# Optimization experiments

Measured on AMD Instinct MI355X. Metric: run time of the kernel, lower is better.

The kernel has to match this reference:

```python
import jax, jax.numpy as jnp
import numpy as np

N_NODES = 50000
N_EDGES = 800000
D_IN = 96
D_HID = 96
D_OUT = 4


def _glorot(key, shape):
    lim = float(np.sqrt(6.0 / (shape[0] + shape[1])))
    return jax.random.uniform(key, shape, jnp.float32, -lim, lim)


def setup_inputs() -> dict:
    key = jax.random.key(0)
    ks = jax.random.split(key, 8)
    x = jax.random.normal(ks[0], (N_NODES, D_IN), jnp.float32)
    edge_index = jax.random.randint(ks[1], (2, N_EDGES), 0, N_NODES, jnp.int64)
    return {
        'x': x,
        'edge_index': edge_index,
        'W0': _glorot(ks[2], (D_IN, D_HID)), 'b0': jnp.zeros((D_HID,), jnp.float32),
        'W1': _glorot(ks[3], (D_HID, D_HID)), 'b1': jnp.zeros((D_HID,), jnp.float32),
        'W2': _glorot(ks[4], (D_HID, D_HID)), 'b2': jnp.zeros((D_HID,), jnp.float32),
        'Wfc': _glorot(ks[5], (D_HID, D_OUT)), 'bfc': jnp.zeros((D_OUT,), jnp.float32),
    }


def _gcn_conv(x, src, dst, W, b, n):
    # GCNConv: linear transform, add self-loops, symmetric degree norm, scatter-add.
    h = x @ W                                   # [N, D]
    loops = jnp.arange(n, dtype=src.dtype)
    s = jnp.concatenate([src, loops])           # [E+N]
    d = jnp.concatenate([dst, loops])
    deg = jax.ops.segment_sum(jnp.ones_like(d, dtype=h.dtype), d, num_segments=n)
    dinv = jnp.where(deg > 0, jax.lax.rsqrt(deg), 0.0)
    norm = dinv[s] * dinv[d]                    # [E+N]
    msgs = h[s] * norm[:, None]                 # gather + scale
    out = jax.ops.segment_sum(msgs, d, num_segments=n)  # scatter-add
    return out + b


def reference(x, edge_index, W0, b0, W1, b1, W2, b2, Wfc, bfc):
    src, dst = edge_index[0], edge_index[1]
    n = x.shape[0]
    h = jax.nn.relu(_gcn_conv(x, src, dst, W0, b0, n))   # dropout = identity (eval)
    h = jax.nn.relu(_gcn_conv(h, src, dst, W1, b1, n))
    h = jax.nn.relu(_gcn_conv(h, src, dst, W2, b2, n))
    return h @ Wfc + bfc
```

## Files before the change

kernel.cpp:

```cpp
#include <hip/hip_runtime.h>

typedef __bf16 bf16x8 __attribute__((ext_vector_type(8)));
typedef float  f32x4  __attribute__((ext_vector_type(4)));
typedef float  f32x8  __attribute__((ext_vector_type(8)));
typedef unsigned short ushort;
typedef ushort us8 __attribute__((ext_vector_type(8)));

constexpr int N_NODES = 50000;
constexpr int N_EDGES = 800000;
constexpr int SLOTS = 64;
constexpr int GE   = N_EDGES / 256;
constexpr int WBLK = (3 * 9216) / 256;
constexpr int GMF  = (N_NODES + 63) / 64;

__device__ inline float h16f(ushort u) {
    union { _Float16 h; ushort u; } cv; cv.u = u; return (float)cv.h;
}
__device__ inline ushort f16b(float f) {
    union { _Float16 h; ushort u; } cv; cv.h = (_Float16)f; return cv.u;
}
__device__ inline ushort bf16b(float f) {
    union { __bf16 b; ushort u; } cv; cv.b = (__bf16)f; return cv.u;
}
__device__ inline f32x8 bf8_to_f32(us8 u) {
    f32x8 r;
#pragma unroll
    for (int i = 0; i < 8; ++i) r[i] = __uint_as_float(((unsigned int)u[i]) << 16);
    return r;
}

__global__ __launch_bounds__(256) void k_count(const int* __restrict__ dst,
                                               int* __restrict__ cnt,
                                               ushort* __restrict__ rank,
                                               const float* __restrict__ W0,
                                               const float* __restrict__ W1,
                                               const float* __restrict__ W2,
                                               ushort* __restrict__ Wt) {
    const int b = blockIdx.x;
    if (b < GE) {
        int e = b * 256 + threadIdx.x;
        rank[e] = (ushort)atomicAdd(&cnt[dst[e]], 1);
    } else {
        int i = (b - GE) * 256 + threadIdx.x;
        int m = i / 9216, li = i - m * 9216;
        const float* W = (m == 0) ? W0 : (m == 1) ? W1 : W2;
        int k = li / 96, c = li - k * 96;
        Wt[m * 9216 + c * 96 + k] = bf16b(W[li]);
    }
}

template<int IN>
__device__ __forceinline__ void gemm_tile(ushort* sX, ushort* sW, const void* Xv,
                                          const ushort* __restrict__ Wt,
                                          ushort* __restrict__ Y, int bt) {
    const int tid = threadIdx.x;
    const int rowbase = bt * 64;

    for (int i = tid; i < 9216 / 8; i += 256)
        ((uint4*)sW)[i] = ((const uint4*)Wt)[i];

    if (IN == 0) {
        const float* X = (const float*)Xv;
        for (int i = tid; i < 64 * 24; i += 256) {
            int r = i / 24, c4 = i % 24;
            int gr = rowbase + r;
            float4 v = make_float4(0.f, 0.f, 0.f, 0.f);
            if (gr < N_NODES) v = ((const float4*)(X + (size_t)gr * 96))[c4];
            ushort* p = sX + r * 96 + c4 * 4;
            p[0] = bf16b(v.x); p[1] = bf16b(v.y); p[2] = bf16b(v.z); p[3] = bf16b(v.w);
        }
    } else {
        const ushort* X = (const ushort*)Xv;
        for (int i = tid; i < 64 * 12; i += 256) {
            int r = i / 12, c8 = i % 12;
            int gr = rowbase + r;
            uint4 v = make_uint4(0, 0, 0, 0);
            if (gr < N_NODES) v = ((const uint4*)(X + (size_t)gr * 96))[c8];
            ((uint4*)(sX + r * 96))[c8] = v;
        }
    }
    __syncthreads();

    const int wv = tid >> 6, lane = tid & 63, quad = lane >> 4, l16 = lane & 15;
    f32x4 acc[6];
#pragma unroll
    for (int t = 0; t < 6; ++t) acc[t] = (f32x4){0.f, 0.f, 0.f, 0.f};

    const ushort* ax = sX + (wv * 16 + l16) * 96 + quad * 8;
#pragma unroll
    for (int s = 0; s < 3; ++s) {
        bf16x8 a = *(const bf16x8*)(ax + s * 32);
#pragma unroll
        for (int t = 0; t < 6; ++t) {
            bf16x8 b = *(const bf16x8*)(sW + (t * 16 + l16) * 96 + s * 32 + quad * 8);
            acc[t] = __builtin_amdgcn_mfma_f32_16x16x32_bf16(a, b, acc[t], 0, 0, 0);
        }
    }
    const int r0 = rowbase + wv * 16 + quad * 4;
#pragma unroll
    for (int t = 0; t < 6; ++t) {
#pragma unroll
        for (int g = 0; g < 4; ++g) {
            int r = r0 + g;
            if (r < N_NODES) Y[(size_t)r * 96 + t * 16 + l16] = bf16b(acc[t][g]);
        }
    }
}

__global__ __launch_bounds__(256) void k_fill_gemm1(const int* __restrict__ src,
                                                    const int* __restrict__ dst,
                                                    const int* __restrict__ cnt,
                                                    const ushort* __restrict__ rank,
                                                    unsigned int* __restrict__ csr,
                                                    const float* __restrict__ x,
                                                    const ushort* __restrict__ Wt,
                                                    ushort* __restrict__ H) {
    __shared__ ushort sS[64 * 96 + 96 * 96];
    const int b = blockIdx.x;
    if (b < GE) {
        int e = b * 256 + threadIdx.x;
        int s = src[e], d = dst[e];
        float hs = rsqrtf((float)(cnt[s] + 1));
        unsigned int entry = (unsigned int)(ushort)s | ((unsigned int)f16b(hs) << 16);
        csr[(size_t)d * SLOTS + rank[e]] = entry;
    } else {
        gemm_tile<0>(sS, sS + 64 * 96, (const void*)x, Wt, H, b - GE);
    }
}

__global__ __launch_bounds__(256) void k_gemm_b(const ushort* __restrict__ X,
                                                const ushort* __restrict__ Wt,
                                                ushort* __restrict__ Y) {
    __shared__ ushort sS[64 * 96 + 96 * 96];
    gemm_tile<1>(sS, sS + 64 * 96, (const void*)X, Wt, Y, blockIdx.x);
}

template<int MODE>
__global__ __launch_bounds__(192) void k_agg(const ushort* __restrict__ A,
                                             const int* __restrict__ cnt,
                                             const unsigned int* __restrict__ csr,
                                             const float* __restrict__ bias,
                                             ushort* __restrict__ Hout,
                                             float* __restrict__ out4,
                                             const float* __restrict__ Wfc,
                                             const float* __restrict__ bfc) {
    __shared__ float sWfc[384];
    __shared__ float red[16][12][4];
    const int tid = threadIdx.x;
    if (MODE == 1) {
        for (int i = tid; i < 384; i += 192) sWfc[i] = Wfc[i];
        __syncthreads();
    }
    const int g = tid / 12, c = tid % 12;
    const int n = blockIdx.x * 16 + g;

    const int deg = cnt[n];
    const float dn = rsqrtf((float)(deg + 1));
    us8 a0 = *(const us8*)(A + (size_t)n * 96 + c * 8);
    f32x8 acc = bf8_to_f32(a0) * (dn * dn);

    const unsigned int* row = csr + (size_t)n * SLOTS;
    int j = 0;
    for (; j + 4 <= deg; j += 4) {
        const uint4 q = *(const uint4*)(row + j);
        const us8 u0 = *(const us8*)(A + (size_t)(q.x & 0xFFFFu) * 96 + c * 8);
        const us8 u1 = *(const us8*)(A + (size_t)(q.y & 0xFFFFu) * 96 + c * 8);
        const us8 u2 = *(const us8*)(A + (size_t)(q.z & 0xFFFFu) * 96 + c * 8);
        const us8 u3 = *(const us8*)(A + (size_t)(q.w & 0xFFFFu) * 96 + c * 8);
        acc += bf8_to_f32(u0) * (h16f((ushort)(q.x >> 16)) * dn);
        acc += bf8_to_f32(u1) * (h16f((ushort)(q.y >> 16)) * dn);
        acc += bf8_to_f32(u2) * (h16f((ushort)(q.z >> 16)) * dn);
        acc += bf8_to_f32(u3) * (h16f((ushort)(q.w >> 16)) * dn);
    }
    for (; j < deg; ++j) {
        const unsigned int e = row[j];
        const float w = h16f((ushort)(e >> 16)) * dn;
        const us8 u = *(const us8*)(A + (size_t)(e & 0xFFFFu) * 96 + c * 8);
        acc += bf8_to_f32(u) * w;
    }
#pragma unroll
    for (int f = 0; f < 8; ++f) acc[f] = fmaxf(acc[f] + bias[c * 8 + f], 0.0f);

    if (MODE == 0) {
        us8 o;
#pragma unroll
        for (int f = 0; f < 8; ++f) o[f] = bf16b(acc[f]);
        *(us8*)(Hout + (size_t)n * 96 + c * 8) = o;
    } else {
        float p0 = 0.f, p1 = 0.f, p2 = 0.f, p3 = 0.f;
#pragma unroll
        for (int f = 0; f < 8; ++f) {
            const float* wr = sWfc + (c * 8 + f) * 4;
            p0 += acc[f] * wr[0];
            p1 += acc[f] * wr[1];
            p2 += acc[f] * wr[2];
            p3 += acc[f] * wr[3];
        }
        red[g][c][0] = p0; red[g][c][1] = p1; red[g][c][2] = p2; red[g][c][3] = p3;
        __syncthreads();
        if (tid < 64) {
            const int gg = tid >> 2, jj = tid & 3;
            float s = bfc[jj];
#pragma unroll
            for (int cc = 0; cc < 12; ++cc) s += red[gg][cc][jj];
            out4[(size_t)(blockIdx.x * 16 + gg) * 4 + jj] = s;
        }
    }
}

extern "C" void kernel_launch(void* const* d_in, const int* in_sizes, int n_in,
                              void* d_out, int out_size, void* d_ws, size_t ws_size,
                              hipStream_t stream) {
    const float* x   = (const float*)d_in[0];
    const int*   ei  = (const int*)d_in[1];
    const int*   src = ei;
    const int*   dst = ei + N_EDGES;
    const float* W0  = (const float*)d_in[2];
    const float* b0  = (const float*)d_in[3];
    const float* W1  = (const float*)d_in[4];
    const float* b1  = (const float*)d_in[5];
    const float* W2  = (const float*)d_in[6];
    const float* b2  = (const float*)d_in[7];
    const float* Wfc = (const float*)d_in[8];
    const float* bfc = (const float*)d_in[9];
    float* out = (float*)d_out;

    char* w = (char*)d_ws;
    unsigned int* csr = (unsigned int*)w;  w += ((size_t)N_NODES * SLOTS * 4 + 15) & ~15ULL;
    int*    cnt  = (int*)w;                w += ((size_t)N_NODES * 4 + 15) & ~15ULL;
    ushort* rank = (ushort*)w;             w += ((size_t)N_EDGES * 2 + 15) & ~15ULL;
    ushort* Wt   = (ushort*)w;             w += ((size_t)3 * 9216 * 2 + 15) & ~15ULL;
    ushort* H    = (ushort*)w;             w += ((size_t)N_NODES * 96 * 2 + 15) & ~15ULL;
    ushort* G    = (ushort*)w;

    const int gAgg = N_NODES / 16;

    hipMemsetAsync(cnt, 0, (size_t)N_NODES * 4, stream);
    hipLaunchKernelGGL(k_count, dim3(GE + WBLK), dim3(256), 0, stream,
                       dst, cnt, rank, W0, W1, W2, Wt);
    hipLaunchKernelGGL(k_fill_gemm1, dim3(GE + GMF), dim3(256), 0, stream,
                       src, dst, cnt, rank, csr, x, Wt, H);
    hipLaunchKernelGGL((k_agg<0>), dim3(gAgg), dim3(192), 0, stream,
                       H, cnt, csr, b0, G, (float*)nullptr,
                       (const float*)nullptr, (const float*)nullptr);
    hipLaunchKernelGGL(k_gemm_b, dim3(GMF), dim3(256), 0, stream, G, Wt + 9216, H);
    hipLaunchKernelGGL((k_agg<0>), dim3(gAgg), dim3(192), 0, stream,
                       H, cnt, csr, b1, G, (float*)nullptr,
                       (const float*)nullptr, (const float*)nullptr);
    hipLaunchKernelGGL(k_gemm_b, dim3(GMF), dim3(256), 0, stream, G, Wt + 2 * 9216, H);
    hipLaunchKernelGGL((k_agg<1>), dim3(gAgg), dim3(192), 0, stream,
                       H, cnt, csr, b2, (ushort*)nullptr, out, Wfc, bfc);
}
```

Baseline: 239.7 us.

## Fuse neighbor aggregation with the next layer's GEMM in one kernel

The per-layer aggregation kernel and the following dense GEMM kernel are merged into a single kernel. Each 256-thread block aggregates 64 nodes (4 threads per node, 24 features each), writes the ReLU output as bf16 into shared memory, then runs the MFMA transform directly from LDS. This removes the global round-trip of the intermediate activations and two kernel launches. In exchange, each thread now walks a whole neighbor list with three 16-byte gathers per neighbor, which lowers parallelism, and 64 rows per block can leave load imbalance across degrees.

```diff
diff --git a/kernel.cpp b/kernel.cpp
--- a/kernel.cpp
+++ b/kernel.cpp
@@ -49,38 +49,9 @@
     }
 }
 
-template<int IN>
-__device__ __forceinline__ void gemm_tile(ushort* sX, ushort* sW, const void* Xv,
-                                          const ushort* __restrict__ Wt,
-                                          ushort* __restrict__ Y, int bt) {
-    const int tid = threadIdx.x;
-    const int rowbase = bt * 64;
-
-    for (int i = tid; i < 9216 / 8; i += 256)
-        ((uint4*)sW)[i] = ((const uint4*)Wt)[i];
-
-    if (IN == 0) {
-        const float* X = (const float*)Xv;
-        for (int i = tid; i < 64 * 24; i += 256) {
-            int r = i / 24, c4 = i % 24;
-            int gr = rowbase + r;
-            float4 v = make_float4(0.f, 0.f, 0.f, 0.f);
-            if (gr < N_NODES) v = ((const float4*)(X + (size_t)gr * 96))[c4];
-            ushort* p = sX + r * 96 + c4 * 4;
-            p[0] = bf16b(v.x); p[1] = bf16b(v.y); p[2] = bf16b(v.z); p[3] = bf16b(v.w);
-        }
-    } else {
-        const ushort* X = (const ushort*)Xv;
-        for (int i = tid; i < 64 * 12; i += 256) {
-            int r = i / 12, c8 = i % 12;
-            int gr = rowbase + r;
-            uint4 v = make_uint4(0, 0, 0, 0);
-            if (gr < N_NODES) v = ((const uint4*)(X + (size_t)gr * 96))[c8];
-            ((uint4*)(sX + r * 96))[c8] = v;
-        }
-    }
-    __syncthreads();
-
+__device__ __forceinline__ void mfma_store(const ushort* sX, const ushort* sW,
+                                           ushort* __restrict__ Y, int rowbase) {
+    const int tid = threadIdx.x;
     const int wv = tid >> 6, lane = tid & 63, quad = lane >> 4, l16 = lane & 15;
     f32x4 acc[6];
 #pragma unroll
@@ -117,40 +88,115 @@
                                                     ushort* __restrict__ H) {
     __shared__ ushort sS[64 * 96 + 96 * 96];
     const int b = blockIdx.x;
+    const int tid = threadIdx.x;
     if (b < GE) {
-        int e = b * 256 + threadIdx.x;
+        int e = b * 256 + tid;
         int s = src[e], d = dst[e];
         float hs = rsqrtf((float)(cnt[s] + 1));
         unsigned int entry = (unsigned int)(ushort)s | ((unsigned int)f16b(hs) << 16);
         csr[(size_t)d * SLOTS + rank[e]] = entry;
     } else {
-        gemm_tile<0>(sS, sS + 64 * 96, (const void*)x, Wt, H, b - GE);
-    }
-}
-
-__global__ __launch_bounds__(256) void k_gemm_b(const ushort* __restrict__ X,
+        ushort* sX = sS;
+        ushort* sW = sS + 64 * 96;
+        const int rowbase = (b - GE) * 64;
+        for (int i = tid; i < 9216 / 8; i += 256)
+            ((uint4*)sW)[i] = ((const uint4*)Wt)[i];
+        for (int i = tid; i < 64 * 24; i += 256) {
+            int r = i / 24, c4 = i % 24;
+            int gr = rowbase + r;
+            float4 v = make_float4(0.f, 0.f, 0.f, 0.f);
+            if (gr < N_NODES) v = ((const float4*)(x + (size_t)gr * 96))[c4];
+            ushort* p = sX + r * 96 + c4 * 4;
+            p[0] = bf16b(v.x); p[1] = bf16b(v.y); p[2] = bf16b(v.z); p[3] = bf16b(v.w);
+        }
+        __syncthreads();
+        mfma_store(sX, sW, H, rowbase);
+    }
+}
+
+__global__ __launch_bounds__(256) void k_aggemm(const ushort* __restrict__ A,
+                                                const int* __restrict__ cnt,
+                                                const unsigned int* __restrict__ csr,
+                                                const float* __restrict__ bias,
                                                 const ushort* __restrict__ Wt,
                                                 ushort* __restrict__ Y) {
     __shared__ ushort sS[64 * 96 + 96 * 96];
-    gemm_tile<1>(sS, sS + 64 * 96, (const void*)X, Wt, Y, blockIdx.x);
-}
-
-template<int MODE>
-__global__ __launch_bounds__(192) void k_agg(const ushort* __restrict__ A,
-                                             const int* __restrict__ cnt,
-                                             const unsigned int* __restrict__ csr,
-                                             const float* __restrict__ bias,
-                                             ushort* __restrict__ Hout,
-                                             float* __restrict__ out4,
-                                             const float* __restrict__ Wfc,
-                                             const float* __restrict__ bfc) {
+    ushort* sX = sS;
+    ushort* sW = sS + 64 * 96;
+    const int tid = threadIdx.x;
+    const int rowbase = blockIdx.x * 64;
+
+    for (int i = tid; i < 9216 / 8; i += 256)
+        ((uint4*)sW)[i] = ((const uint4*)Wt)[i];
+
+    const int nl = tid >> 2;
+    const int grp = tid & 3;
+    const int n = rowbase + nl;
+    if (n < N_NODES) {
+        const int deg = cnt[n];
+        const float dn = rsqrtf((float)(deg + 1));
+        const float dn2 = dn * dn;
+        const ushort* An = A + (size_t)n * 96 + grp * 24;
+        f32x8 acc0 = bf8_to_f32(*(const us8*)(An))      * dn2;
+        f32x8 acc1 = bf8_to_f32(*(const us8*)(An + 8))  * dn2;
+        f32x8 acc2 = bf8_to_f32(*(const us8*)(An + 16)) * dn2;
+
+        const unsigned int* row = csr + (size_t)n * SLOTS;
+        int j = 0;
+        for (; j + 4 <= deg; j += 4) {
+            const uint4 q = *(const uint4*)(row + j);
+            const ushort* p0 = A + (size_t)(q.x & 0xFFFFu) * 96 + grp * 24;
+            const ushort* p1 = A + (size_t)(q.y & 0xFFFFu) * 96 + grp * 24;
+            const ushort* p2 = A + (size_t)(q.z & 0xFFFFu) * 96 + grp * 24;
+            const ushort* p3 = A + (size_t)(q.w & 0xFFFFu) * 96 + grp * 24;
+            const us8 u00 = *(const us8*)p0, u01 = *(const us8*)(p0 + 8), u02 = *(const us8*)(p0 + 16);
+            const us8 u10 = *(const us8*)p1, u11 = *(const us8*)(p1 + 8), u12 = *(const us8*)(p1 + 16);
+            const us8 u20 = *(const us8*)p2, u21 = *(const us8*)(p2 + 8), u22 = *(const us8*)(p2 + 16);
+            const us8 u30 = *(const us8*)p3, u31 = *(const us8*)(p3 + 8), u32 = *(const us8*)(p3 + 16);
+            const float w0 = h16f((ushort)(q.x >> 16)) * dn;
+            const float w1 = h16f((ushort)(q.y >> 16)) * dn;
+            const float w2 = h16f((ushort)(q.z >> 16)) * dn;
+            const float w3 = h16f((ushort)(q.w >> 16)) * dn;
+            acc0 += bf8_to_f32(u00) * w0; acc1 += bf8_to_f32(u01) * w0; acc2 += bf8_to_f32(u02) * w0;
+            acc0 += bf8_to_f32(u10) * w1; acc1 += bf8_to_f32(u11) * w1; acc2 += bf8_to_f32(u12) * w1;
+            acc0 += bf8_to_f32(u20) * w2; acc1 += bf8_to_f32(u21) * w2; acc2 += bf8_to_f32(u22) * w2;
+            acc0 += bf8_to_f32(u30) * w3; acc1 += bf8_to_f32(u31) * w3; acc2 += bf8_to_f32(u32) * w3;
+        }
+        for (; j < deg; ++j) {
+            const unsigned int e = row[j];
+            const float w = h16f((ushort)(e >> 16)) * dn;
+            const ushort* p = A + (size_t)(e & 0xFFFFu) * 96 + grp * 24;
+            acc0 += bf8_to_f32(*(const us8*)p) * w;
+            acc1 += bf8_to_f32(*(const us8*)(p + 8)) * w;
+            acc2 += bf8_to_f32(*(const us8*)(p + 16)) * w;
+        }
+        const float* bp = bias + grp * 24;
+        us8 o0, o1, o2;
+#pragma unroll
+        for (int f = 0; f < 8; ++f) {
+            o0[f] = bf16b(fmaxf(acc0[f] + bp[f],      0.0f));
+            o1[f] = bf16b(fmaxf(acc1[f] + bp[8 + f],  0.0f));
+            o2[f] = bf16b(fmaxf(acc2[f] + bp[16 + f], 0.0f));
+        }
+        ushort* sxp = sX + nl * 96 + grp * 24;
+        *(us8*)sxp = o0; *(us8*)(sxp + 8) = o1; *(us8*)(sxp + 16) = o2;
+    }
+    __syncthreads();
+    mfma_store(sX, sW, Y, rowbase);
+}
+
+__global__ __launch_bounds__(192) void k_agg_fc(const ushort* __restrict__ A,
+                                                const int* __restrict__ cnt,
+                                                const unsigned int* __restrict__ csr,
+                                                const float* __restrict__ bias,
+                                                float* __restrict__ out4,
+                                                const float* __restrict__ Wfc,
+                                                const float* __restrict__ bfc) {
     __shared__ float sWfc[384];
     __shared__ float red[16][12][4];
     const int tid = threadIdx.x;
-    if (MODE == 1) {
-        for (int i = tid; i < 384; i += 192) sWfc[i] = Wfc[i];
-        __syncthreads();
-    }
+    for (int i = tid; i < 384; i += 192) sWfc[i] = Wfc[i];
+    __syncthreads();
     const int g = tid / 12, c = tid % 12;
     const int n = blockIdx.x * 16 + g;
 
@@ -181,30 +227,23 @@
 #pragma unroll
     for (int f = 0; f < 8; ++f) acc[f] = fmaxf(acc[f] + bias[c * 8 + f], 0.0f);
 
-    if (MODE == 0) {
-        us8 o;
-#pragma unroll
-        for (int f = 0; f < 8; ++f) o[f] = bf16b(acc[f]);
-        *(us8*)(Hout + (size_t)n * 96 + c * 8) = o;
-    } else {
-        float p0 = 0.f, p1 = 0.f, p2 = 0.f, p3 = 0.f;
-#pragma unroll
-        for (int f = 0; f < 8; ++f) {
-            const float* wr = sWfc + (c * 8 + f) * 4;
-            p0 += acc[f] * wr[0];
-            p1 += acc[f] * wr[1];
-            p2 += acc[f] * wr[2];
-            p3 += acc[f] * wr[3];
-        }
-        red[g][c][0] = p0; red[g][c][1] = p1; red[g][c][2] = p2; red[g][c][3] = p3;
-        __syncthreads();
-        if (tid < 64) {
-            const int gg = tid >> 2, jj = tid & 3;
-            float s = bfc[jj];
-#pragma unroll
-            for (int cc = 0; cc < 12; ++cc) s += red[gg][cc][jj];
-            out4[(size_t)(blockIdx.x * 16 + gg) * 4 + jj] = s;
-        }
+    float p0 = 0.f, p1 = 0.f, p2 = 0.f, p3 = 0.f;
+#pragma unroll
+    for (int f = 0; f < 8; ++f) {
+        const float* wr = sWfc + (c * 8 + f) * 4;
+        p0 += acc[f] * wr[0];
+        p1 += acc[f] * wr[1];
+        p2 += acc[f] * wr[2];
+        p3 += acc[f] * wr[3];
+    }
+    red[g][c][0] = p0; red[g][c][1] = p1; red[g][c][2] = p2; red[g][c][3] = p3;
+    __syncthreads();
+    if (tid < 64) {
+        const int gg = tid >> 2, jj = tid & 3;
+        float s = bfc[jj];
+#pragma unroll
+        for (int cc = 0; cc < 12; ++cc) s += red[gg][cc][jj];
+        out4[(size_t)(blockIdx.x * 16 + gg) * 4 + jj] = s;
     }
 }
 
@@ -240,14 +279,10 @@
                        dst, cnt, rank, W0, W1, W2, Wt);
     hipLaunchKernelGGL(k_fill_gemm1, dim3(GE + GMF), dim3(256), 0, stream,
                        src, dst, cnt, rank, csr, x, Wt, H);
-    hipLaunchKernelGGL((k_agg<0>), dim3(gAgg), dim3(192), 0, stream,
-                       H, cnt, csr, b0, G, (float*)nullptr,
-                       (const float*)nullptr, (const float*)nullptr);
-    hipLaunchKernelGGL(k_gemm_b, dim3(GMF), dim3(256), 0, stream, G, Wt + 9216, H);
-    hipLaunchKernelGGL((k_agg<0>), dim3(gAgg), dim3(192), 0, stream,
-                       H, cnt, csr, b1, G, (float*)nullptr,
-                       (const float*)nullptr, (const float*)nullptr);
-    hipLaunchKernelGGL(k_gemm_b, dim3(GMF), dim3(256), 0, stream, G, Wt + 2 * 9216, H);
-    hipLaunchKernelGGL((k_agg<1>), dim3(gAgg), dim3(192), 0, stream,
-                       H, cnt, csr, b2, (ushort*)nullptr, out, Wfc, bfc);
-}
+    hipLaunchKernelGGL(k_aggemm, dim3(GMF), dim3(256), 0, stream,
+                       H, cnt, csr, b0, Wt + 9216, G);
+    hipLaunchKernelGGL(k_aggemm, dim3(GMF), dim3(256), 0, stream,
+                       G, cnt, csr, b1, Wt + 2 * 9216, H);
+    hipLaunchKernelGGL(k_agg_fc, dim3(gAgg), dim3(192), 0, stream,
+                       H, cnt, csr, b2, out, Wfc, bfc);
+}
```

Result: no change. 239.0 us (-0.3%).
